# Performance work log

Hardware: AMD Instinct MI355X
Metric: run time of the kernel (lower is better)

The kernel has to match this reference:

```python
import jax, jax.numpy as jnp
import numpy as np

V, E_DIM, H, B, T = 390, 256, 512, 64, 512
START = 388


def setup_inputs() -> dict:
    key = jax.random.key(0)
    ks = jax.random.split(key, 32)
    s = 0.05
    rn = lambda k, shape: jax.random.normal(k, shape, jnp.float32) * s
    inp = {
        "input": jax.random.normal(ks[0], (B, T, V), jnp.float32),
        # encoder params
        "enc_emb": rn(ks[1], (V, E_DIM)),
        "enc_Wih0": rn(ks[2], (3 * H, E_DIM)),
        "enc_Whh0": rn(ks[3], (3 * H, H)),
        "enc_bih0": rn(ks[4], (3 * H,)),
        "enc_bhh0": rn(ks[5], (3 * H,)),
        "enc_Wih1": rn(ks[6], (3 * H, H)),
        "enc_Whh1": rn(ks[7], (3 * H, H)),
        "enc_bih1": rn(ks[8], (3 * H,)),
        "enc_bhh1": rn(ks[9], (3 * H,)),
        # decoder params
        "dec_emb": rn(ks[10], (V, E_DIM)),
        "dec_Wih0": rn(ks[11], (3 * H, E_DIM)),
        "dec_Whh0": rn(ks[12], (3 * H, H)),
        "dec_bih0": rn(ks[13], (3 * H,)),
        "dec_bhh0": rn(ks[14], (3 * H,)),
        "dec_Wih1": rn(ks[15], (3 * H, H)),
        "dec_Whh1": rn(ks[16], (3 * H, H)),
        "dec_bih1": rn(ks[17], (3 * H,)),
        "dec_bhh1": rn(ks[18], (3 * H,)),
        # prediction head
        "Wp1": rn(ks[19], (H, H)),
        "bp1": rn(ks[20], (H,)),
        "Wp2": rn(ks[21], (V, H)),
        "bp2": rn(ks[22], (V,)),
    }
    return inp


def _gru_cell(x, h, Wih, Whh, bih, bhh):
    # PyTorch GRU cell: gates ordered (r, z, n)
    gi = x @ Wih.T + bih
    gh = h @ Whh.T + bhh
    ir, iz, inn = jnp.split(gi, 3, axis=-1)
    hr, hz, hn = jnp.split(gh, 3, axis=-1)
    r = jax.nn.sigmoid(ir + hr)
    z = jax.nn.sigmoid(iz + hz)
    n = jnp.tanh(inn + r * hn)
    return (1.0 - z) * n + z * h


def reference(input, enc_emb, enc_Wih0, enc_Whh0, enc_bih0, enc_bhh0,
              enc_Wih1, enc_Whh1, enc_bih1, enc_bhh1,
              dec_emb, dec_Wih0, dec_Whh0, dec_bih0, dec_bhh0,
              dec_Wih1, dec_Whh1, dec_bih1, dec_bhh1,
              Wp1, bp1, Wp2, bp2):
    batch, max_len, vocab = input.shape
    hdim = enc_Whh0.shape[1]

    # ---- Encoder: soft embedding + 2-layer GRU, keep final hidden states ----
    x = jnp.einsum('btv,ve->bte', input, enc_emb)  # [B,T,E]
    xt = jnp.transpose(x, (1, 0, 2))               # time-major [T,B,E]
    h0 = jnp.zeros((batch, hdim), input.dtype)

    def step0(h, xt_):
        h = _gru_cell(xt_, h, enc_Wih0, enc_Whh0, enc_bih0, enc_bhh0)
        return h, h
    h1_enc, seq1 = jax.lax.scan(step0, h0, xt)

    def step1(h, xt_):
        h = _gru_cell(xt_, h, enc_Wih1, enc_Whh1, enc_bih1, enc_bhh1)
        return h, None
    h2_enc, _ = jax.lax.scan(step1, h0, seq1)

    tok0 = jnp.full((batch,), START, jnp.int32)
    rng0 = jax.random.key(42)

    def dec_step(carry, _):
        h1, h2, tok, rng = carry
        rng, sk = jax.random.split(rng)
        xe = dec_emb[tok]                               # [B,E]
        h1 = _gru_cell(xe, h1, dec_Wih0, dec_Whh0, dec_bih0, dec_bhh0)
        h2 = _gru_cell(h1, h2, dec_Wih1, dec_Whh1, dec_bih1, dec_bhh1)
        hid = h2 @ Wp1.T + bp1
        hid = jnp.where(hid >= 0, hid, 0.1 * hid)       # LeakyReLU(0.1)
        logits = hid @ Wp2.T + bp2                      # temp=1 -> logits/temp == logits
        probs = jax.nn.softmax(logits, axis=-1)
        tok = jax.random.categorical(sk, logits, axis=-1).astype(jnp.int32)
        return (h1, h2, tok, rng), (probs, tok)

    _, (probs_seq, toks) = jax.lax.scan(
        dec_step, (h1_enc, h2_enc, tok0, rng0), None, length=max_len - 1)

    start_oh = jax.nn.one_hot(tok0, vocab, dtype=input.dtype)  # [B,V]
    outputs = jnp.concatenate(
        [start_oh[:, None, :], jnp.transpose(probs_seq, (1, 0, 2))], axis=1)
    max_output = jnp.concatenate(
        [jnp.full((batch, 1), float(START), jnp.float32),
         toks.T.astype(jnp.float32)], axis=1)
    return outputs, max_output
```

## Files before the change

kernel.cpp:

```cpp
#include <hip/hip_runtime.h>
#include <math.h>


#define BB 64
#define TT 512
#define VV 390
#define EE 256
#define HH 512

static __device__ __forceinline__ void tf2x32(unsigned k0, unsigned k1,
                                              unsigned x0, unsigned x1,
                                              unsigned &o0, unsigned &o1) {
  unsigned ks2 = k0 ^ k1 ^ 0x1BD11BDAu;
  x0 += k0; x1 += k1;
#define TFR(r) x0 += x1; x1 = (x1 << (r)) | (x1 >> (32 - (r))); x1 ^= x0;
  TFR(13) TFR(15) TFR(26) TFR(6)
  x0 += k1; x1 += ks2 + 1u;
  TFR(17) TFR(29) TFR(16) TFR(24)
  x0 += ks2; x1 += k0 + 2u;
  TFR(13) TFR(15) TFR(26) TFR(6)
  x0 += k0; x1 += k1 + 3u;
  TFR(17) TFR(29) TFR(16) TFR(24)
  x0 += k1; x1 += ks2 + 4u;
  TFR(13) TFR(15) TFR(26) TFR(6)
  x0 += ks2; x1 += k0 + 5u;
#undef TFR
  o0 = x0; o1 = x1;
}

static __device__ __forceinline__ float sigm(float x) {
  return 1.0f / (1.0f + expf(-x));
}

template <int K>
static __device__ __forceinline__ void dot3_kb(const float* __restrict__ X, int b,
    const float* __restrict__ w0, const float* __restrict__ w1,
    const float* __restrict__ w2, float &r0, float &r1, float &r2) {
  const float4* q0 = (const float4*)w0;
  const float4* q1 = (const float4*)w1;
  const float4* q2 = (const float4*)w2;
  float s0 = 0.f, s1 = 0.f, s2 = 0.f;
#pragma unroll 4
  for (int k4 = 0; k4 < (K >> 2); ++k4) {
    float4 u0 = q0[k4], u1 = q1[k4], u2 = q2[k4];
    int kb = (k4 << 8) + b;
    float x0 = X[kb], x1 = X[kb + 64], x2 = X[kb + 128], x3 = X[kb + 192];
    s0 = fmaf(x0, u0.x, s0); s0 = fmaf(x1, u0.y, s0); s0 = fmaf(x2, u0.z, s0); s0 = fmaf(x3, u0.w, s0);
    s1 = fmaf(x0, u1.x, s1); s1 = fmaf(x1, u1.y, s1); s1 = fmaf(x2, u1.z, s1); s1 = fmaf(x3, u1.w, s1);
    s2 = fmaf(x0, u2.x, s2); s2 = fmaf(x1, u2.y, s2); s2 = fmaf(x2, u2.z, s2); s2 = fmaf(x3, u2.w, s2);
  }
  r0 = s0; r1 = s1; r2 = s2;
}

template <int K>
static __device__ __forceinline__ void dot3_row(const float* __restrict__ xrow,
    const float* __restrict__ w0, const float* __restrict__ w1,
    const float* __restrict__ w2, float &r0, float &r1, float &r2) {
  const float4* xq = (const float4*)xrow;
  const float4* q0 = (const float4*)w0;
  const float4* q1 = (const float4*)w1;
  const float4* q2 = (const float4*)w2;
  float s0 = 0.f, s1 = 0.f, s2 = 0.f;
#pragma unroll 4
  for (int k4 = 0; k4 < (K >> 2); ++k4) {
    float4 x = xq[k4];
    float4 u0 = q0[k4], u1 = q1[k4], u2 = q2[k4];
    s0 = fmaf(x.x, u0.x, s0); s0 = fmaf(x.y, u0.y, s0); s0 = fmaf(x.z, u0.z, s0); s0 = fmaf(x.w, u0.w, s0);
    s1 = fmaf(x.x, u1.x, s1); s1 = fmaf(x.y, u1.y, s1); s1 = fmaf(x.z, u1.z, s1); s1 = fmaf(x.w, u1.w, s1);
    s2 = fmaf(x.x, u2.x, s2); s2 = fmaf(x.y, u2.y, s2); s2 = fmaf(x.z, u2.z, s2); s2 = fmaf(x.w, u2.w, s2);
  }
  r0 = s0; r1 = s1; r2 = s2;
}

__global__ __launch_bounds__(256) void k_init(float* __restrict__ out,
    float* __restrict__ h1buf, float* __restrict__ h2buf,
    int* __restrict__ tok, unsigned* __restrict__ rng) {
  int wg = blockIdx.x, tid = threadIdx.x;
  for (int i = wg * 256 + tid; i < HH * BB; i += 64 * 256) {
    h1buf[i] = 0.f;
    h2buf[i] = 0.f;
  }
  for (int v = tid; v < VV; v += 256)
    out[(size_t)wg * TT * VV + v] = (v == 388) ? 1.0f : 0.0f;
  if (tid == 0) {
    out[(size_t)BB * TT * VV + (size_t)wg * TT] = 388.0f;
    tok[wg] = 388;
    if (wg == 0) { rng[0] = 0u; rng[1] = 42u; rng[2] = 0u; rng[3] = 0u; }
  }
}

__global__ __launch_bounds__(256) void k_xgemm(const float* __restrict__ input,
    const float* __restrict__ emb, float* __restrict__ xT) {
  int t = blockIdx.x, tid = threadIdx.x;
  int s = tid >> 6, b = tid & 63;
  __shared__ float lin[64 * 65];
  float4 acc[16];
#pragma unroll
  for (int i = 0; i < 16; ++i) acc[i] = make_float4(0.f, 0.f, 0.f, 0.f);
  for (int k0 = 0; k0 < VV; k0 += 64) {
    int kmax = min(64, VV - k0);
    __syncthreads();
#pragma unroll
    for (int r = 0; r < 16; ++r) {
      int idx = r * 256 + tid;
      int b2 = idx >> 6, kk = idx & 63;
      if (kk < kmax)
        lin[kk * 65 + b2] = input[((size_t)b2 * TT + t) * VV + k0 + kk];
    }
    __syncthreads();
    for (int kk = 0; kk < kmax; ++kk) {
      float xv = lin[kk * 65 + b];
      const float4* er = (const float4*)(emb + (size_t)(k0 + kk) * EE);
#pragma unroll
      for (int i = 0; i < 16; ++i) {
        float4 w = er[s + 4 * i];
        acc[i].x = fmaf(xv, w.x, acc[i].x);
        acc[i].y = fmaf(xv, w.y, acc[i].y);
        acc[i].z = fmaf(xv, w.z, acc[i].z);
        acc[i].w = fmaf(xv, w.w, acc[i].w);
      }
    }
  }
  float* dst0 = xT + (size_t)t * (EE * 64);
#pragma unroll
  for (int i = 0; i < 16; ++i) {
    int e = (s + 4 * i) * 4;
    float* d = dst0 + e * 64 + b;
    d[0] = acc[i].x; d[64] = acc[i].y; d[128] = acc[i].z; d[192] = acc[i].w;
  }
}

__global__ __launch_bounds__(256) void k_enc_step(int t,
    const float* __restrict__ xT, float* __restrict__ h1buf, float* __restrict__ h2buf,
    const float* __restrict__ Wih0, const float* __restrict__ Whh0,
    const float* __restrict__ bih0, const float* __restrict__ bhh0,
    const float* __restrict__ Wih1, const float* __restrict__ Whh1,
    const float* __restrict__ bih1, const float* __restrict__ bhh1) {
  int wg = blockIdx.x, tid = threadIdx.x;
  int s = tid >> 6, b = tid & 63;
  const float* h1_r = h1buf + (t & 1) * (HH * BB);
  float* h1_w = h1buf + ((t + 1) & 1) * (HH * BB);
  if (wg < 128) {
    if (t >= TT) return;
    int j = wg * 4 + s;
    float ar, az, an, hr, hz, hn;
    dot3_kb<EE>(xT + (size_t)t * (EE * 64), b,
                Wih0 + (size_t)j * EE, Wih0 + (size_t)(512 + j) * EE,
                Wih0 + (size_t)(1024 + j) * EE, ar, az, an);
    dot3_kb<HH>(h1_r, b,
                Whh0 + (size_t)j * HH, Whh0 + (size_t)(512 + j) * HH,
                Whh0 + (size_t)(1024 + j) * HH, hr, hz, hn);
    float r = sigm((ar + bih0[j]) + (hr + bhh0[j]));
    float z = sigm((az + bih0[512 + j]) + (hz + bhh0[512 + j]));
    float n = tanhf((an + bih0[1024 + j]) + r * (hn + bhh0[1024 + j]));
    h1_w[j * 64 + b] = (1.0f - z) * n + z * h1_r[j * 64 + b];
  } else {
    if (t < 1) return;
    int j = (wg - 128) * 4 + s;
    const float* h2_r = h2buf + ((t + 1) & 1) * (HH * BB);
    float* h2_w = h2buf + (t & 1) * (HH * BB);
    float ar, az, an, hr, hz, hn;
    dot3_kb<HH>(h1_r, b,
                Wih1 + (size_t)j * HH, Wih1 + (size_t)(512 + j) * HH,
                Wih1 + (size_t)(1024 + j) * HH, ar, az, an);
    dot3_kb<HH>(h2_r, b,
                Whh1 + (size_t)j * HH, Whh1 + (size_t)(512 + j) * HH,
                Whh1 + (size_t)(1024 + j) * HH, hr, hz, hn);
    float r = sigm((ar + bih1[j]) + (hr + bhh1[j]));
    float z = sigm((az + bih1[512 + j]) + (hz + bhh1[512 + j]));
    float n = tanhf((an + bih1[1024 + j]) + r * (hn + bhh1[1024 + j]));
    h2_w[j * 64 + b] = (1.0f - z) * n + z * h2_r[j * 64 + b];
  }
}

__global__ __launch_bounds__(256) void k_decA(int d, float* __restrict__ h1buf,
    const float* __restrict__ demb, const float* __restrict__ Wih,
    const float* __restrict__ Whh, const float* __restrict__ bih,
    const float* __restrict__ bhh, const int* __restrict__ tok) {
  int wg = blockIdx.x, tid = threadIdx.x, s = tid >> 6, b = tid & 63;
  const float* h1_r = h1buf + (d & 1) * (HH * BB);
  float* h1_w = h1buf + ((d + 1) & 1) * (HH * BB);
  int j = wg * 4 + s;
  int tk = tok[b];
  float ar, az, an, hr, hz, hn;
  dot3_row<EE>(demb + (size_t)tk * EE,
               Wih + (size_t)j * EE, Wih + (size_t)(512 + j) * EE,
               Wih + (size_t)(1024 + j) * EE, ar, az, an);
  dot3_kb<HH>(h1_r, b,
              Whh + (size_t)j * HH, Whh + (size_t)(512 + j) * HH,
              Whh + (size_t)(1024 + j) * HH, hr, hz, hn);
  float r = sigm((ar + bih[j]) + (hr + bhh[j]));
  float z = sigm((az + bih[512 + j]) + (hz + bhh[512 + j]));
  float n = tanhf((an + bih[1024 + j]) + r * (hn + bhh[1024 + j]));
  h1_w[j * 64 + b] = (1.0f - z) * n + z * h1_r[j * 64 + b];
}

__global__ __launch_bounds__(256) void k_decB(int d, const float* __restrict__ h1buf,
    float* __restrict__ h2buf, const float* __restrict__ Wih,
    const float* __restrict__ Whh, const float* __restrict__ bih,
    const float* __restrict__ bhh) {
  int wg = blockIdx.x, tid = threadIdx.x, s = tid >> 6, b = tid & 63;
  const float* h1n = h1buf + ((d + 1) & 1) * (HH * BB);
  const float* h2r = h2buf + (d & 1) * (HH * BB);
  float* h2w = h2buf + ((d + 1) & 1) * (HH * BB);
  int j = wg * 4 + s;
  float ar, az, an, hr, hz, hn;
  dot3_kb<HH>(h1n, b,
              Wih + (size_t)j * HH, Wih + (size_t)(512 + j) * HH,
              Wih + (size_t)(1024 + j) * HH, ar, az, an);
  dot3_kb<HH>(h2r, b,
              Whh + (size_t)j * HH, Whh + (size_t)(512 + j) * HH,
              Whh + (size_t)(1024 + j) * HH, hr, hz, hn);
  float r = sigm((ar + bih[j]) + (hr + bhh[j]));
  float z = sigm((az + bih[512 + j]) + (hz + bhh[512 + j]));
  float n = tanhf((an + bih[1024 + j]) + r * (hn + bhh[1024 + j]));
  h2w[j * 64 + b] = (1.0f - z) * n + z * h2r[j * 64 + b];
}

__global__ __launch_bounds__(256) void k_decC(int d, const float* __restrict__ h2buf,
    const float* __restrict__ Wp1, const float* __restrict__ bp1,
    const float* __restrict__ Wp2, const float* __restrict__ bp2,
    float* __restrict__ out, int* __restrict__ tok, unsigned* __restrict__ rng) {
  __shared__ __align__(16) float lh[HH];
  __shared__ __align__(16) float lhid[HH];
  __shared__ float lv[VV];
  __shared__ float rf[8];
  __shared__ int ri[4];
  int b = blockIdx.x, tid = threadIdx.x;
  const float* h2 = h2buf + ((d + 1) & 1) * (HH * BB);
  lh[tid] = h2[tid * 64 + b];
  lh[tid + 256] = h2[(tid + 256) * 64 + b];
  __syncthreads();
  for (int c = tid; c < HH; c += 256) {
    const float4* w = (const float4*)(Wp1 + (size_t)c * HH);
    float a = 0.f;
#pragma unroll 4
    for (int k4 = 0; k4 < HH / 4; ++k4) {
      float4 q = w[k4];
      float4 hv = *(const float4*)&lh[k4 * 4];
      a = fmaf(hv.x, q.x, a); a = fmaf(hv.y, q.y, a);
      a = fmaf(hv.z, q.z, a); a = fmaf(hv.w, q.w, a);
    }
    a += bp1[c];
    lhid[c] = (a >= 0.f) ? a : 0.1f * a;
  }
  __syncthreads();
  for (int c = tid; c < VV; c += 256) {
    const float4* w = (const float4*)(Wp2 + (size_t)c * HH);
    float a = 0.f;
#pragma unroll 4
    for (int k4 = 0; k4 < HH / 4; ++k4) {
      float4 q = w[k4];
      float4 hv = *(const float4*)&lhid[k4 * 4];
      a = fmaf(hv.x, q.x, a); a = fmaf(hv.y, q.y, a);
      a = fmaf(hv.z, q.z, a); a = fmaf(hv.w, q.w, a);
    }
    lv[c] = a + bp2[c];
  }
  __syncthreads();
  float m = -INFINITY;
  for (int c = tid; c < VV; c += 256) m = fmaxf(m, lv[c]);
  for (int off = 32; off > 0; off >>= 1) m = fmaxf(m, __shfl_down(m, off, 64));
  if ((tid & 63) == 0) rf[tid >> 6] = m;
  __syncthreads();
  if (tid == 0) rf[4] = fmaxf(fmaxf(rf[0], rf[1]), fmaxf(rf[2], rf[3]));
  __syncthreads();
  m = rf[4];
  unsigned k0r = rng[(d & 1) * 2], k1r = rng[(d & 1) * 2 + 1];
  unsigned sk0, sk1;
  tf2x32(k0r, k1r, 0u, 1u, sk0, sk1);
  float by = -INFINITY; int bc = 0x7fffffff;
  for (int c = tid; c < VV; c += 256) {
    unsigned o0, o1;
    tf2x32(sk0, sk1, 0u, (unsigned)(b * VV + c), o0, o1);
    unsigned bits = o0 ^ o1;
    float f = __uint_as_float(0x3f800000u | (bits >> 9)) - 1.0f;
    float u = (f > 0.f) ? f : 1.17549435e-38f;
    float g = (float)(-log(-log((double)u)));
    float y = lv[c] + g;
    if (y > by || (y == by && c < bc)) { by = y; bc = c; }
  }
  for (int off = 32; off > 0; off >>= 1) {
    float oy = __shfl_down(by, off, 64);
    int oc = __shfl_down(bc, off, 64);
    if (oy > by || (oy == by && oc < bc)) { by = oy; bc = oc; }
  }
  if ((tid & 63) == 0) { rf[tid >> 6] = by; ri[tid >> 6] = bc; }
  __syncthreads();
  if (tid == 0) {
    by = rf[0]; bc = ri[0];
    for (int w2 = 1; w2 < 4; ++w2)
      if (rf[w2] > by || (rf[w2] == by && ri[w2] < bc)) { by = rf[w2]; bc = ri[w2]; }
    tok[b] = bc;
    out[(size_t)BB * TT * VV + (size_t)b * TT + (d + 1)] = (float)bc;
    if (b == 0) {
      unsigned n0, n1;
      tf2x32(k0r, k1r, 0u, 0u, n0, n1);
      rng[((d + 1) & 1) * 2] = n0;
      rng[((d + 1) & 1) * 2 + 1] = n1;
    }
  }
  __syncthreads();
  float e0 = 0.f, e1 = 0.f, ssum = 0.f;
  {
    int c = tid;
    if (c < VV) { e0 = expf(lv[c] - m); ssum += e0; }
    c = tid + 256;
    if (c < VV) { e1 = expf(lv[c] - m); ssum += e1; }
  }
  for (int off = 32; off > 0; off >>= 1) ssum += __shfl_down(ssum, off, 64);
  if ((tid & 63) == 0) rf[tid >> 6] = ssum;
  __syncthreads();
  if (tid == 0) rf[4] = (rf[0] + rf[1]) + (rf[2] + rf[3]);
  __syncthreads();
  float S = rf[4];
  float* orow = out + ((size_t)b * TT + (d + 1)) * VV;
  if (tid < VV) orow[tid] = e0 / S;
  if (tid + 256 < VV) orow[tid + 256] = e1 / S;
}

extern "C" void kernel_launch(void* const* d_in, const int* in_sizes, int n_in,
                              void* d_out, int out_size, void* d_ws, size_t ws_size,
                              hipStream_t stream) {
  (void)in_sizes; (void)n_in; (void)out_size; (void)ws_size;
  const float* input = (const float*)d_in[0];
  const float* e_emb = (const float*)d_in[1];
  const float* eWih0 = (const float*)d_in[2];
  const float* eWhh0 = (const float*)d_in[3];
  const float* ebih0 = (const float*)d_in[4];
  const float* ebhh0 = (const float*)d_in[5];
  const float* eWih1 = (const float*)d_in[6];
  const float* eWhh1 = (const float*)d_in[7];
  const float* ebih1 = (const float*)d_in[8];
  const float* ebhh1 = (const float*)d_in[9];
  const float* d_emb = (const float*)d_in[10];
  const float* dWih0 = (const float*)d_in[11];
  const float* dWhh0 = (const float*)d_in[12];
  const float* dbih0 = (const float*)d_in[13];
  const float* dbhh0 = (const float*)d_in[14];
  const float* dWih1 = (const float*)d_in[15];
  const float* dWhh1 = (const float*)d_in[16];
  const float* dbih1 = (const float*)d_in[17];
  const float* dbhh1 = (const float*)d_in[18];
  const float* Wp1   = (const float*)d_in[19];
  const float* bp1   = (const float*)d_in[20];
  const float* Wp2   = (const float*)d_in[21];
  const float* bp2   = (const float*)d_in[22];
  float* out = (float*)d_out;

  float* xT = (float*)d_ws;
  float* h1buf = xT + (size_t)TT * EE * 64;
  float* h2buf = h1buf + 2 * HH * BB;
  int* tok = (int*)(h2buf + 2 * HH * BB);
  unsigned* rng = (unsigned*)(tok + 64);

  k_init<<<64, 256, 0, stream>>>(out, h1buf, h2buf, tok, rng);
  k_xgemm<<<TT, 256, 0, stream>>>(input, e_emb, xT);
  for (int t = 0; t <= TT; ++t)
    k_enc_step<<<256, 256, 0, stream>>>(t, xT, h1buf, h2buf,
        eWih0, eWhh0, ebih0, ebhh0, eWih1, eWhh1, ebih1, ebhh1);
  for (int d = 0; d < TT - 1; ++d) {
    k_decA<<<128, 256, 0, stream>>>(d, h1buf, d_emb, dWih0, dWhh0, dbih0, dbhh0, tok);
    k_decB<<<128, 256, 0, stream>>>(d, h1buf, h2buf, dWih1, dWhh1, dbih1, dbhh1);
    k_decC<<<64, 256, 0, stream>>>(d, h2buf, Wp1, bp1, Wp2, bp2, out, tok, rng);
  }
}
```

Measured before the change: 85.75 ms.

## Fuse encoder/decoder steps into one persistent kernel with grid barriers and LDS-resident weights

Replaces roughly 2000 per-timestep kernel launches with a single persistent kernel of 256 workgroups. A hierarchical atomic grid barrier separates the steps. Each workgroup caches its slice of all GRU weight rows in shared memory (about 90KB) and reuses it across every timestep. Decoder embedding lookup is moved into the sampling phase, which writes a transposed embedding buffer. The risks are deadlock if all 256 workgroups cannot be co-resident, spin-barrier overhead, and lower occupancy from the large LDS allocation.

```diff
diff --git a/kernel.cpp b/kernel.cpp
--- a/kernel.cpp
+++ b/kernel.cpp
@@ -7,6 +7,7 @@
 #define VV 390
 #define EE 256
 #define HH 512
+#define NTHR 256
 
 static __device__ __forceinline__ void tf2x32(unsigned k0, unsigned k1,
                                               unsigned x0, unsigned x1,
@@ -52,29 +53,27 @@
   r0 = s0; r1 = s1; r2 = s2;
 }
 
-template <int K>
-static __device__ __forceinline__ void dot3_row(const float* __restrict__ xrow,
-    const float* __restrict__ w0, const float* __restrict__ w1,
-    const float* __restrict__ w2, float &r0, float &r1, float &r2) {
-  const float4* xq = (const float4*)xrow;
-  const float4* q0 = (const float4*)w0;
-  const float4* q1 = (const float4*)w1;
-  const float4* q2 = (const float4*)w2;
-  float s0 = 0.f, s1 = 0.f, s2 = 0.f;
-#pragma unroll 4
-  for (int k4 = 0; k4 < (K >> 2); ++k4) {
-    float4 x = xq[k4];
-    float4 u0 = q0[k4], u1 = q1[k4], u2 = q2[k4];
-    s0 = fmaf(x.x, u0.x, s0); s0 = fmaf(x.y, u0.y, s0); s0 = fmaf(x.z, u0.z, s0); s0 = fmaf(x.w, u0.w, s0);
-    s1 = fmaf(x.x, u1.x, s1); s1 = fmaf(x.y, u1.y, s1); s1 = fmaf(x.z, u1.z, s1); s1 = fmaf(x.w, u1.w, s1);
-    s2 = fmaf(x.x, u2.x, s2); s2 = fmaf(x.y, u2.y, s2); s2 = fmaf(x.z, u2.z, s2); s2 = fmaf(x.w, u2.w, s2);
-  }
-  r0 = s0; r1 = s1; r2 = s2;
+static __device__ __forceinline__ void gbar(unsigned* bar, unsigned gen, int wg) {
+  __syncthreads();
+  if (threadIdx.x == 0) {
+    unsigned tgt = gen * 16u;
+    unsigned* grp = bar + 32 + (wg >> 4) * 32;
+    __hip_atomic_fetch_add(grp, 1u, __ATOMIC_RELEASE, __HIP_MEMORY_SCOPE_AGENT);
+    if ((wg & 15) == 0) {
+      while (__hip_atomic_load(grp, __ATOMIC_ACQUIRE, __HIP_MEMORY_SCOPE_AGENT) < tgt)
+        __builtin_amdgcn_s_sleep(1);
+      __hip_atomic_fetch_add(bar, 1u, __ATOMIC_RELEASE, __HIP_MEMORY_SCOPE_AGENT);
+    }
+    while (__hip_atomic_load(bar, __ATOMIC_ACQUIRE, __HIP_MEMORY_SCOPE_AGENT) < tgt)
+      __builtin_amdgcn_s_sleep(1);
+  }
+  __syncthreads();
 }
 
 __global__ __launch_bounds__(256) void k_init(float* __restrict__ out,
     float* __restrict__ h1buf, float* __restrict__ h2buf,
-    int* __restrict__ tok, unsigned* __restrict__ rng) {
+    float* __restrict__ xeT, unsigned* __restrict__ rng,
+    unsigned* __restrict__ bar, const float* __restrict__ demb) {
   int wg = blockIdx.x, tid = threadIdx.x;
   for (int i = wg * 256 + tid; i < HH * BB; i += 64 * 256) {
     h1buf[i] = 0.f;
@@ -82,11 +81,13 @@
   }
   for (int v = tid; v < VV; v += 256)
     out[(size_t)wg * TT * VV + v] = (v == 388) ? 1.0f : 0.0f;
+  xeT[tid * 64 + wg] = demb[388 * EE + tid];
   if (tid == 0) {
     out[(size_t)BB * TT * VV + (size_t)wg * TT] = 388.0f;
-    tok[wg] = 388;
     if (wg == 0) { rng[0] = 0u; rng[1] = 42u; rng[2] = 0u; rng[3] = 0u; }
   }
+  if (wg == 0)
+    for (int i = tid; i < 544; i += 256) bar[i] = 0u;
 }
 
 __global__ __launch_bounds__(256) void k_xgemm(const float* __restrict__ input,
@@ -130,193 +131,232 @@
   }
 }
 
-__global__ __launch_bounds__(256) void k_enc_step(int t,
+__global__ __launch_bounds__(256) void k_seq(
     const float* __restrict__ xT, float* __restrict__ h1buf, float* __restrict__ h2buf,
-    const float* __restrict__ Wih0, const float* __restrict__ Whh0,
-    const float* __restrict__ bih0, const float* __restrict__ bhh0,
-    const float* __restrict__ Wih1, const float* __restrict__ Whh1,
-    const float* __restrict__ bih1, const float* __restrict__ bhh1) {
-  int wg = blockIdx.x, tid = threadIdx.x;
-  int s = tid >> 6, b = tid & 63;
-  const float* h1_r = h1buf + (t & 1) * (HH * BB);
-  float* h1_w = h1buf + ((t + 1) & 1) * (HH * BB);
-  if (wg < 128) {
-    if (t >= TT) return;
-    int j = wg * 4 + s;
-    float ar, az, an, hr, hz, hn;
-    dot3_kb<EE>(xT + (size_t)t * (EE * 64), b,
-                Wih0 + (size_t)j * EE, Wih0 + (size_t)(512 + j) * EE,
-                Wih0 + (size_t)(1024 + j) * EE, ar, az, an);
-    dot3_kb<HH>(h1_r, b,
-                Whh0 + (size_t)j * HH, Whh0 + (size_t)(512 + j) * HH,
-                Whh0 + (size_t)(1024 + j) * HH, hr, hz, hn);
-    float r = sigm((ar + bih0[j]) + (hr + bhh0[j]));
-    float z = sigm((az + bih0[512 + j]) + (hz + bhh0[512 + j]));
-    float n = tanhf((an + bih0[1024 + j]) + r * (hn + bhh0[1024 + j]));
-    h1_w[j * 64 + b] = (1.0f - z) * n + z * h1_r[j * 64 + b];
-  } else {
-    if (t < 1) return;
-    int j = (wg - 128) * 4 + s;
-    const float* h2_r = h2buf + ((t + 1) & 1) * (HH * BB);
-    float* h2_w = h2buf + (t & 1) * (HH * BB);
-    float ar, az, an, hr, hz, hn;
-    dot3_kb<HH>(h1_r, b,
-                Wih1 + (size_t)j * HH, Wih1 + (size_t)(512 + j) * HH,
-                Wih1 + (size_t)(1024 + j) * HH, ar, az, an);
-    dot3_kb<HH>(h2_r, b,
-                Whh1 + (size_t)j * HH, Whh1 + (size_t)(512 + j) * HH,
-                Whh1 + (size_t)(1024 + j) * HH, hr, hz, hn);
-    float r = sigm((ar + bih1[j]) + (hr + bhh1[j]));
-    float z = sigm((az + bih1[512 + j]) + (hz + bhh1[512 + j]));
-    float n = tanhf((an + bih1[1024 + j]) + r * (hn + bhh1[1024 + j]));
-    h2_w[j * 64 + b] = (1.0f - z) * n + z * h2_r[j * 64 + b];
-  }
-}
-
-__global__ __launch_bounds__(256) void k_decA(int d, float* __restrict__ h1buf,
-    const float* __restrict__ demb, const float* __restrict__ Wih,
-    const float* __restrict__ Whh, const float* __restrict__ bih,
-    const float* __restrict__ bhh, const int* __restrict__ tok) {
-  int wg = blockIdx.x, tid = threadIdx.x, s = tid >> 6, b = tid & 63;
-  const float* h1_r = h1buf + (d & 1) * (HH * BB);
-  float* h1_w = h1buf + ((d + 1) & 1) * (HH * BB);
-  int j = wg * 4 + s;
-  int tk = tok[b];
-  float ar, az, an, hr, hz, hn;
-  dot3_row<EE>(demb + (size_t)tk * EE,
-               Wih + (size_t)j * EE, Wih + (size_t)(512 + j) * EE,
-               Wih + (size_t)(1024 + j) * EE, ar, az, an);
-  dot3_kb<HH>(h1_r, b,
-              Whh + (size_t)j * HH, Whh + (size_t)(512 + j) * HH,
-              Whh + (size_t)(1024 + j) * HH, hr, hz, hn);
-  float r = sigm((ar + bih[j]) + (hr + bhh[j]));
-  float z = sigm((az + bih[512 + j]) + (hz + bhh[512 + j]));
-  float n = tanhf((an + bih[1024 + j]) + r * (hn + bhh[1024 + j]));
-  h1_w[j * 64 + b] = (1.0f - z) * n + z * h1_r[j * 64 + b];
-}
-
-__global__ __launch_bounds__(256) void k_decB(int d, const float* __restrict__ h1buf,
-    float* __restrict__ h2buf, const float* __restrict__ Wih,
-    const float* __restrict__ Whh, const float* __restrict__ bih,
-    const float* __restrict__ bhh) {
-  int wg = blockIdx.x, tid = threadIdx.x, s = tid >> 6, b = tid & 63;
-  const float* h1n = h1buf + ((d + 1) & 1) * (HH * BB);
-  const float* h2r = h2buf + (d & 1) * (HH * BB);
-  float* h2w = h2buf + ((d + 1) & 1) * (HH * BB);
-  int j = wg * 4 + s;
-  float ar, az, an, hr, hz, hn;
-  dot3_kb<HH>(h1n, b,
-              Wih + (size_t)j * HH, Wih + (size_t)(512 + j) * HH,
-              Wih + (size_t)(1024 + j) * HH, ar, az, an);
-  dot3_kb<HH>(h2r, b,
-              Whh + (size_t)j * HH, Whh + (size_t)(512 + j) * HH,
-              Whh + (size_t)(1024 + j) * HH, hr, hz, hn);
-  float r = sigm((ar + bih[j]) + (hr + bhh[j]));
-  float z = sigm((az + bih[512 + j]) + (hz + bhh[512 + j]));
-  float n = tanhf((an + bih[1024 + j]) + r * (hn + bhh[1024 + j]));
-  h2w[j * 64 + b] = (1.0f - z) * n + z * h2r[j * 64 + b];
-}
-
-__global__ __launch_bounds__(256) void k_decC(int d, const float* __restrict__ h2buf,
+    float* __restrict__ xeT, unsigned* __restrict__ rng, unsigned* __restrict__ bar,
+    const float* __restrict__ eWih0, const float* __restrict__ eWhh0,
+    const float* __restrict__ ebih0, const float* __restrict__ ebhh0,
+    const float* __restrict__ eWih1, const float* __restrict__ eWhh1,
+    const float* __restrict__ ebih1, const float* __restrict__ ebhh1,
+    const float* __restrict__ demb,
+    const float* __restrict__ dWih0, const float* __restrict__ dWhh0,
+    const float* __restrict__ dbih0, const float* __restrict__ dbhh0,
+    const float* __restrict__ dWih1, const float* __restrict__ dWhh1,
+    const float* __restrict__ dbih1, const float* __restrict__ dbhh1,
     const float* __restrict__ Wp1, const float* __restrict__ bp1,
     const float* __restrict__ Wp2, const float* __restrict__ bp2,
-    float* __restrict__ out, int* __restrict__ tok, unsigned* __restrict__ rng) {
-  __shared__ __align__(16) float lh[HH];
-  __shared__ __align__(16) float lhid[HH];
-  __shared__ float lv[VV];
-  __shared__ float rf[8];
-  __shared__ int ri[4];
-  int b = blockIdx.x, tid = threadIdx.x;
-  const float* h2 = h2buf + ((d + 1) & 1) * (HH * BB);
-  lh[tid] = h2[tid * 64 + b];
-  lh[tid + 256] = h2[(tid + 256) * 64 + b];
+    float* __restrict__ out) {
+  extern __shared__ float smem[];
+  int wg = blockIdx.x, tid = threadIdx.x;
+  int wv = tid >> 6, b = tid & 63;
+  float* scr = smem + 21504;
+
+  for (int u = 0; u < 2; ++u) {
+    int j = 2 * wg + u;
+    for (int g = 0; g < 3; ++g) {
+      float* d0 = smem + u * 2304 + g * 768;
+      const float* s0 = eWih0 + (size_t)(g * 512 + j) * EE;
+      for (int i = tid; i < EE; i += NTHR) d0[i] = s0[i];
+      const float* s1 = eWhh0 + (size_t)(g * 512 + j) * HH;
+      for (int i = tid; i < HH; i += NTHR) d0[EE + i] = s1[i];
+      float* d1 = smem + 4608 + u * 3072 + g * 1024;
+      const float* s2 = eWih1 + (size_t)(g * 512 + j) * HH;
+      for (int i = tid; i < HH; i += NTHR) d1[i] = s2[i];
+      const float* s3 = eWhh1 + (size_t)(g * 512 + j) * HH;
+      for (int i = tid; i < HH; i += NTHR) d1[HH + i] = s3[i];
+      float* d2 = smem + 10752 + u * 2304 + g * 768;
+      const float* s4 = dWih0 + (size_t)(g * 512 + j) * EE;
+      for (int i = tid; i < EE; i += NTHR) d2[i] = s4[i];
+      const float* s5 = dWhh0 + (size_t)(g * 512 + j) * HH;
+      for (int i = tid; i < HH; i += NTHR) d2[EE + i] = s5[i];
+      float* d3 = smem + 15360 + u * 3072 + g * 1024;
+      const float* s6 = dWih1 + (size_t)(g * 512 + j) * HH;
+      for (int i = tid; i < HH; i += NTHR) d3[i] = s6[i];
+      const float* s7 = dWhh1 + (size_t)(g * 512 + j) * HH;
+      for (int i = tid; i < HH; i += NTHR) d3[HH + i] = s7[i];
+    }
+  }
   __syncthreads();
-  for (int c = tid; c < HH; c += 256) {
-    const float4* w = (const float4*)(Wp1 + (size_t)c * HH);
-    float a = 0.f;
+  unsigned gen = 0;
+
+  for (int t = 0; t <= TT; ++t) {
+    bool isL1 = (wv >= 2);
+    bool act = isL1 ? (t >= 1) : (t < TT);
+    if (act) {
+      int j = 2 * wg + (wv & 1);
+      const float* h1r = h1buf + (t & 1) * (HH * BB);
+      if (!isL1) {
+        const float* wb = smem + (wv & 1) * 2304;
+        float ax0, ax1, ax2, ah0, ah1, ah2;
+        dot3_kb<EE>(xT + (size_t)t * (EE * 64), b, wb, wb + 768, wb + 1536, ax0, ax1, ax2);
+        dot3_kb<HH>(h1r, b, wb + EE, wb + 768 + EE, wb + 1536 + EE, ah0, ah1, ah2);
+        float r = sigm((ax0 + ebih0[j]) + (ah0 + ebhh0[j]));
+        float z = sigm((ax1 + ebih0[512 + j]) + (ah1 + ebhh0[512 + j]));
+        float n = tanhf((ax2 + ebih0[1024 + j]) + r * (ah2 + ebhh0[1024 + j]));
+        float* h1w = h1buf + ((t + 1) & 1) * (HH * BB);
+        h1w[j * 64 + b] = (1.0f - z) * n + z * h1r[j * 64 + b];
+      } else {
+        const float* wb = smem + 4608 + (wv & 1) * 3072;
+        const float* h2r = h2buf + ((t + 1) & 1) * (HH * BB);
+        float ax0, ax1, ax2, ah0, ah1, ah2;
+        dot3_kb<HH>(h1r, b, wb, wb + 1024, wb + 2048, ax0, ax1, ax2);
+        dot3_kb<HH>(h2r, b, wb + HH, wb + 1024 + HH, wb + 2048 + HH, ah0, ah1, ah2);
+        float r = sigm((ax0 + ebih1[j]) + (ah0 + ebhh1[j]));
+        float z = sigm((ax1 + ebih1[512 + j]) + (ah1 + ebhh1[512 + j]));
+        float n = tanhf((ax2 + ebih1[1024 + j]) + r * (ah2 + ebhh1[1024 + j]));
+        float* h2w = h2buf + (t & 1) * (HH * BB);
+        h2w[j * 64 + b] = (1.0f - z) * n + z * h2r[j * 64 + b];
+      }
+    }
+    gbar(bar, ++gen, wg);
+  }
+
+  for (int d = 0; d < TT - 1; ++d) {
+    const float* h1r = h1buf + (d & 1) * (HH * BB);
+    float* h1w = h1buf + ((d + 1) & 1) * (HH * BB);
+    const float* h2r = h2buf + (d & 1) * (HH * BB);
+    float* h2w = h2buf + ((d + 1) & 1) * (HH * BB);
+
+    {
+      int unit = wv & 1, part = wv >> 1;
+      const float* wb = smem + 10752 + unit * 2304;
+      float a0, a1, a2;
+      if (part == 0) dot3_kb<EE>(xeT, b, wb, wb + 768, wb + 1536, a0, a1, a2);
+      else           dot3_kb<HH>(h1r, b, wb + EE, wb + 768 + EE, wb + 1536 + EE, a0, a1, a2);
+      int pb = ((unit * 2 + part) * 3) * 64 + b;
+      scr[pb] = a0; scr[pb + 64] = a1; scr[pb + 128] = a2;
+      __syncthreads();
+      if (tid < 128) {
+        int u2 = tid >> 6, b2 = tid & 63, j2 = 2 * wg + u2;
+        float ax0 = scr[(u2 * 6 + 0) * 64 + b2], ax1 = scr[(u2 * 6 + 1) * 64 + b2], ax2 = scr[(u2 * 6 + 2) * 64 + b2];
+        float ah0 = scr[(u2 * 6 + 3) * 64 + b2], ah1 = scr[(u2 * 6 + 4) * 64 + b2], ah2 = scr[(u2 * 6 + 5) * 64 + b2];
+        float r = sigm((ax0 + dbih0[j2]) + (ah0 + dbhh0[j2]));
+        float z = sigm((ax1 + dbih0[512 + j2]) + (ah1 + dbhh0[512 + j2]));
+        float n = tanhf((ax2 + dbih0[1024 + j2]) + r * (ah2 + dbhh0[1024 + j2]));
+        h1w[j2 * 64 + b2] = (1.0f - z) * n + z * h1r[j2 * 64 + b2];
+      }
+    }
+    gbar(bar, ++gen, wg);
+
+    {
+      int unit = wv & 1, part = wv >> 1;
+      const float* wb = smem + 15360 + unit * 3072;
+      float a0, a1, a2;
+      if (part == 0) dot3_kb<HH>(h1w, b, wb, wb + 1024, wb + 2048, a0, a1, a2);
+      else           dot3_kb<HH>(h2r, b, wb + HH, wb + 1024 + HH, wb + 2048 + HH, a0, a1, a2);
+      int pb = ((unit * 2 + part) * 3) * 64 + b;
+      scr[pb] = a0; scr[pb + 64] = a1; scr[pb + 128] = a2;
+      __syncthreads();
+      if (tid < 128) {
+        int u2 = tid >> 6, b2 = tid & 63, j2 = 2 * wg + u2;
+        float ax0 = scr[(u2 * 6 + 0) * 64 + b2], ax1 = scr[(u2 * 6 + 1) * 64 + b2], ax2 = scr[(u2 * 6 + 2) * 64 + b2];
+        float ah0 = scr[(u2 * 6 + 3) * 64 + b2], ah1 = scr[(u2 * 6 + 4) * 64 + b2], ah2 = scr[(u2 * 6 + 5) * 64 + b2];
+        float r = sigm((ax0 + dbih1[j2]) + (ah0 + dbhh1[j2]));
+        float z = sigm((ax1 + dbih1[512 + j2]) + (ah1 + dbhh1[512 + j2]));
+        float n = tanhf((ax2 + dbih1[1024 + j2]) + r * (ah2 + dbhh1[1024 + j2]));
+        h2w[j2 * 64 + b2] = (1.0f - z) * n + z * h2r[j2 * 64 + b2];
+      }
+    }
+    gbar(bar, ++gen, wg);
+
+    if (wg < 64) {
+      float* lh = scr; float* lhid = scr + 512; float* lv = scr + 1024;
+      float* rf = scr + 1414; int* ri = (int*)(scr + 1422); int* tokp = (int*)(scr + 1430);
+      int brow = wg;
+      lh[tid] = h2w[tid * 64 + brow];
+      lh[tid + 256] = h2w[(tid + 256) * 64 + brow];
+      __syncthreads();
+      for (int c = tid; c < HH; c += 256) {
+        const float4* w = (const float4*)(Wp1 + (size_t)c * HH);
+        float a = 0.f;
 #pragma unroll 4
-    for (int k4 = 0; k4 < HH / 4; ++k4) {
-      float4 q = w[k4];
-      float4 hv = *(const float4*)&lh[k4 * 4];
-      a = fmaf(hv.x, q.x, a); a = fmaf(hv.y, q.y, a);
-      a = fmaf(hv.z, q.z, a); a = fmaf(hv.w, q.w, a);
-    }
-    a += bp1[c];
-    lhid[c] = (a >= 0.f) ? a : 0.1f * a;
-  }
-  __syncthreads();
-  for (int c = tid; c < VV; c += 256) {
-    const float4* w = (const float4*)(Wp2 + (size_t)c * HH);
-    float a = 0.f;
+        for (int k4 = 0; k4 < HH / 4; ++k4) {
+          float4 q = w[k4];
+          float4 hv = *(const float4*)&lh[k4 * 4];
+          a = fmaf(hv.x, q.x, a); a = fmaf(hv.y, q.y, a);
+          a = fmaf(hv.z, q.z, a); a = fmaf(hv.w, q.w, a);
+        }
+        a += bp1[c];
+        lhid[c] = (a >= 0.f) ? a : 0.1f * a;
+      }
+      __syncthreads();
+      for (int c = tid; c < VV; c += 256) {
+        const float4* w = (const float4*)(Wp2 + (size_t)c * HH);
+        float a = 0.f;
 #pragma unroll 4
-    for (int k4 = 0; k4 < HH / 4; ++k4) {
-      float4 q = w[k4];
-      float4 hv = *(const float4*)&lhid[k4 * 4];
-      a = fmaf(hv.x, q.x, a); a = fmaf(hv.y, q.y, a);
-      a = fmaf(hv.z, q.z, a); a = fmaf(hv.w, q.w, a);
-    }
-    lv[c] = a + bp2[c];
-  }
-  __syncthreads();
-  float m = -INFINITY;
-  for (int c = tid; c < VV; c += 256) m = fmaxf(m, lv[c]);
-  for (int off = 32; off > 0; off >>= 1) m = fmaxf(m, __shfl_down(m, off, 64));
-  if ((tid & 63) == 0) rf[tid >> 6] = m;
-  __syncthreads();
-  if (tid == 0) rf[4] = fmaxf(fmaxf(rf[0], rf[1]), fmaxf(rf[2], rf[3]));
-  __syncthreads();
-  m = rf[4];
-  unsigned k0r = rng[(d & 1) * 2], k1r = rng[(d & 1) * 2 + 1];
-  unsigned sk0, sk1;
-  tf2x32(k0r, k1r, 0u, 1u, sk0, sk1);
-  float by = -INFINITY; int bc = 0x7fffffff;
-  for (int c = tid; c < VV; c += 256) {
-    unsigned o0, o1;
-    tf2x32(sk0, sk1, 0u, (unsigned)(b * VV + c), o0, o1);
-    unsigned bits = o0 ^ o1;
-    float f = __uint_as_float(0x3f800000u | (bits >> 9)) - 1.0f;
-    float u = (f > 0.f) ? f : 1.17549435e-38f;
-    float g = (float)(-log(-log((double)u)));
-    float y = lv[c] + g;
-    if (y > by || (y == by && c < bc)) { by = y; bc = c; }
-  }
-  for (int off = 32; off > 0; off >>= 1) {
-    float oy = __shfl_down(by, off, 64);
-    int oc = __shfl_down(bc, off, 64);
-    if (oy > by || (oy == by && oc < bc)) { by = oy; bc = oc; }
-  }
-  if ((tid & 63) == 0) { rf[tid >> 6] = by; ri[tid >> 6] = bc; }
-  __syncthreads();
-  if (tid == 0) {
-    by = rf[0]; bc = ri[0];
-    for (int w2 = 1; w2 < 4; ++w2)
-      if (rf[w2] > by || (rf[w2] == by && ri[w2] < bc)) { by = rf[w2]; bc = ri[w2]; }
-    tok[b] = bc;
-    out[(size_t)BB * TT * VV + (size_t)b * TT + (d + 1)] = (float)bc;
-    if (b == 0) {
-      unsigned n0, n1;
-      tf2x32(k0r, k1r, 0u, 0u, n0, n1);
-      rng[((d + 1) & 1) * 2] = n0;
-      rng[((d + 1) & 1) * 2 + 1] = n1;
-    }
-  }
-  __syncthreads();
-  float e0 = 0.f, e1 = 0.f, ssum = 0.f;
-  {
-    int c = tid;
-    if (c < VV) { e0 = expf(lv[c] - m); ssum += e0; }
-    c = tid + 256;
-    if (c < VV) { e1 = expf(lv[c] - m); ssum += e1; }
-  }
-  for (int off = 32; off > 0; off >>= 1) ssum += __shfl_down(ssum, off, 64);
-  if ((tid & 63) == 0) rf[tid >> 6] = ssum;
-  __syncthreads();
-  if (tid == 0) rf[4] = (rf[0] + rf[1]) + (rf[2] + rf[3]);
-  __syncthreads();
-  float S = rf[4];
-  float* orow = out + ((size_t)b * TT + (d + 1)) * VV;
-  if (tid < VV) orow[tid] = e0 / S;
-  if (tid + 256 < VV) orow[tid + 256] = e1 / S;
+        for (int k4 = 0; k4 < HH / 4; ++k4) {
+          float4 q = w[k4];
+          float4 hv = *(const float4*)&lhid[k4 * 4];
+          a = fmaf(hv.x, q.x, a); a = fmaf(hv.y, q.y, a);
+          a = fmaf(hv.z, q.z, a); a = fmaf(hv.w, q.w, a);
+        }
+        lv[c] = a + bp2[c];
+      }
+      __syncthreads();
+      float m = -INFINITY;
+      for (int c = tid; c < VV; c += 256) m = fmaxf(m, lv[c]);
+      for (int off = 32; off > 0; off >>= 1) m = fmaxf(m, __shfl_down(m, off, 64));
+      if ((tid & 63) == 0) rf[tid >> 6] = m;
+      __syncthreads();
+      if (tid == 0) rf[4] = fmaxf(fmaxf(rf[0], rf[1]), fmaxf(rf[2], rf[3]));
+      __syncthreads();
+      m = rf[4];
+      unsigned k0r = rng[(d & 1) * 2], k1r = rng[(d & 1) * 2 + 1];
+      unsigned sk0, sk1;
+      tf2x32(k0r, k1r, 0u, 1u, sk0, sk1);
+      float by = -INFINITY; int bc = 0x7fffffff;
+      for (int c = tid; c < VV; c += 256) {
+        unsigned o0, o1;
+        tf2x32(sk0, sk1, 0u, (unsigned)(brow * VV + c), o0, o1);
+        unsigned bits = o0 ^ o1;
+        float f = __uint_as_float(0x3f800000u | (bits >> 9)) - 1.0f;
+        float u = (f > 0.f) ? f : 1.17549435e-38f;
+        float g = (float)(-log(-log((double)u)));
+        float y = lv[c] + g;
+        if (y > by || (y == by && c < bc)) { by = y; bc = c; }
+      }
+      for (int off = 32; off > 0; off >>= 1) {
+        float oy = __shfl_down(by, off, 64);
+        int oc = __shfl_down(bc, off, 64);
+        if (oy > by || (oy == by && oc < bc)) { by = oy; bc = oc; }
+      }
+      if ((tid & 63) == 0) { rf[tid >> 6] = by; ri[tid >> 6] = bc; }
+      __syncthreads();
+      if (tid == 0) {
+        by = rf[0]; bc = ri[0];
+        for (int w2 = 1; w2 < 4; ++w2)
+          if (rf[w2] > by || (rf[w2] == by && ri[w2] < bc)) { by = rf[w2]; bc = ri[w2]; }
+        *tokp = bc;
+        out[(size_t)BB * TT * VV + (size_t)brow * TT + (d + 1)] = (float)bc;
+        if (brow == 0) {
+          unsigned n0, n1;
+          tf2x32(k0r, k1r, 0u, 0u, n0, n1);
+          rng[((d + 1) & 1) * 2] = n0;
+          rng[((d + 1) & 1) * 2 + 1] = n1;
+        }
+      }
+      __syncthreads();
+      int tkn = *tokp;
+      xeT[tid * 64 + brow] = demb[(size_t)tkn * EE + tid];
+      float e0 = 0.f, e1 = 0.f, ssum = 0.f;
+      {
+        int c = tid;
+        if (c < VV) { e0 = expf(lv[c] - m); ssum += e0; }
+        c = tid + 256;
+        if (c < VV) { e1 = expf(lv[c] - m); ssum += e1; }
+      }
+      for (int off = 32; off > 0; off >>= 1) ssum += __shfl_down(ssum, off, 64);
+      if ((tid & 63) == 0) rf[tid >> 6] = ssum;
+      __syncthreads();
+      if (tid == 0) rf[4] = (rf[0] + rf[1]) + (rf[2] + rf[3]);
+      __syncthreads();
+      float S = rf[4];
+      float* orow = out + ((size_t)brow * TT + (d + 1)) * VV;
+      if (tid < VV) orow[tid] = e0 / S;
+      if (tid + 256 < VV) orow[tid + 256] = e1 / S;
+    }
+    gbar(bar, ++gen, wg);
+  }
 }
 
 extern "C" void kernel_launch(void* const* d_in, const int* in_sizes, int n_in,
@@ -351,17 +391,15 @@
   float* xT = (float*)d_ws;
   float* h1buf = xT + (size_t)TT * EE * 64;
   float* h2buf = h1buf + 2 * HH * BB;
-  int* tok = (int*)(h2buf + 2 * HH * BB);
-  unsigned* rng = (unsigned*)(tok + 64);
-
-  k_init<<<64, 256, 0, stream>>>(out, h1buf, h2buf, tok, rng);
+  float* xeT = h2buf + 2 * HH * BB;
+  unsigned* rng = (unsigned*)(xeT + EE * BB);
+  unsigned* bar = rng + 16;
+
+  k_init<<<64, 256, 0, stream>>>(out, h1buf, h2buf, xeT, rng, bar, d_emb);
   k_xgemm<<<TT, 256, 0, stream>>>(input, e_emb, xT);
-  for (int t = 0; t <= TT; ++t)
-    k_enc_step<<<256, 256, 0, stream>>>(t, xT, h1buf, h2buf,
-        eWih0, eWhh0, ebih0, ebhh0, eWih1, eWhh1, ebih1, ebhh1);
-  for (int d = 0; d < TT - 1; ++d) {
-    k_decA<<<128, 256, 0, stream>>>(d, h1buf, d_emb, dWih0, dWhh0, dbih0, dbhh0, tok);
-    k_decB<<<128, 256, 0, stream>>>(d, h1buf, h2buf, dWih1, dWhh1, dbih1, dbhh1);
-    k_decC<<<64, 256, 0, stream>>>(d, h2buf, Wp1, bp1, Wp2, bp2, out, tok, rng);
-  }
-}
+  k_seq<<<256, 256, 23040 * sizeof(float), stream>>>(
+      xT, h1buf, h2buf, xeT, rng, bar,
+      eWih0, eWhh0, ebih0, ebhh0, eWih1, eWhh1, ebih1, ebhh1,
+      d_emb, dWih0, dWhh0, dbih0, dbhh0, dWih1, dWhh1, dbih1, dbhh1,
+      Wp1, bp1, Wp2, bp2, out);
+}
```

Result: slower. 206.3 ms (+140.6%).
